# Optimization experiments

Measured on AMD Instinct MI355X. Metric: run time of the kernel, lower is better.

## Reference

```python
import jax, jax.numpy as jnp
import numpy as np

H = 4096      # hidden_size
NH = 32       # num heads
HD = H // NH  # head_dim = 128
I = 11008     # intermediate_size
T = 2048      # num tokens (single prompt sequence)
G = 128       # AWQ group size
EPS = 1e-6
ROPE_BASE = 10000.0


def _make_qlinear(key, k_in, n_out):
    k1, k2, k3 = jax.random.split(key, 3)
    qw = jax.random.randint(k1, (k_in, n_out), 0, 16, dtype=jnp.int32)
    qz = jax.random.randint(k2, (k_in // G, n_out), 0, 16, dtype=jnp.int32)
    scales = jax.random.uniform(k3, (k_in // G, n_out), dtype=jnp.float32) * 0.01 + 1e-3
    return qw, scales, qz


def setup_inputs() -> dict:
    key = jax.random.key(0)
    ks = jax.random.split(key, 8)
    inp = {
        "positions": jnp.arange(T, dtype=jnp.int64),
        "hidden_states": jax.random.normal(ks[0], (T, H), dtype=jnp.float32),
        "input_ln_w": jnp.ones((H,), dtype=jnp.float32),
        "post_ln_w": jnp.ones((H,), dtype=jnp.float32),
    }
    inp["qkv_qw"], inp["qkv_scales"], inp["qkv_qz"] = _make_qlinear(ks[1], H, 3 * H)
    inp["o_qw"], inp["o_scales"], inp["o_qz"] = _make_qlinear(ks[2], H, H)
    inp["gu_qw"], inp["gu_scales"], inp["gu_qz"] = _make_qlinear(ks[3], H, 2 * I)
    inp["down_qw"], inp["down_scales"], inp["down_qz"] = _make_qlinear(ks[4], I, H)
    return inp


def rms_norm(x, w):
    var = jnp.mean(x * x, axis=-1, keepdims=True)
    return x * jax.lax.rsqrt(var + EPS) * w


def awq_linear(x, qw, scales, qz):
    # dequant: (q - z) * scale, group-wise along K; then dense GEMM
    w = (qw.astype(scales.dtype) - jnp.repeat(qz.astype(scales.dtype), G, axis=0)) \
        * jnp.repeat(scales, G, axis=0)
    return x @ w


def apply_rope(x, positions):
    # x: [T, NH, HD], neox-style half rotation, rotary_dim = HD
    inv_freq = 1.0 / (ROPE_BASE ** (jnp.arange(0, HD, 2, dtype=jnp.float32) / HD))
    ang = positions.astype(jnp.float32)[:, None] * inv_freq  # [T, HD/2]
    cos = jnp.cos(ang)[:, None, :]
    sin = jnp.sin(ang)[:, None, :]
    x1, x2 = x[..., : HD // 2], x[..., HD // 2:]
    return jnp.concatenate([x1 * cos - x2 * sin, x2 * cos + x1 * sin], axis=-1)


def reference(positions, hidden_states, input_ln_w, post_ln_w,
              qkv_qw, qkv_scales, qkv_qz, o_qw, o_scales, o_qz,
              gu_qw, gu_scales, gu_qz, down_qw, down_scales, down_qz):
    residual = hidden_states
    x = rms_norm(hidden_states, input_ln_w)

    # attention
    qkv = awq_linear(x, qkv_qw, qkv_scales, qkv_qz)  # [T, 3H]
    q, k, v = jnp.split(qkv, 3, axis=-1)
    q = apply_rope(q.reshape(T, NH, HD), positions)
    k = apply_rope(k.reshape(T, NH, HD), positions)
    v = v.reshape(T, NH, HD)
    scale = HD ** -0.5
    scores = jnp.einsum('qhd,khd->hqk', q, k) * scale  # [NH, T, T]
    causal = jnp.tril(jnp.ones((T, T), dtype=bool))
    scores = jnp.where(causal[None], scores, jnp.finfo(scores.dtype).min)
    probs = jax.nn.softmax(scores, axis=-1)
    attn = jnp.einsum('hqk,khd->qhd', probs, v).reshape(T, H)
    attn_out = awq_linear(attn, o_qw, o_scales, o_qz)

    hidden = residual + attn_out
    residual = hidden
    x = rms_norm(hidden, post_ln_w)

    # MLP: gate_up -> silu(gate) * up -> down
    gate_up = awq_linear(x, gu_qw, gu_scales, gu_qz)  # [T, 2I]
    gate, up = jnp.split(gate_up, 2, axis=-1)
    x = jax.nn.silu(gate) * up
    x = awq_linear(x, down_qw, down_scales, down_qz)
    return residual + x
```

## Files before the change

### kernel.cpp

```cpp
#include <hip/hip_runtime.h>
#include <stdint.h>

#define T_SEQ 2048
#define HID 4096
#define NHEADS 32
#define I_FF 11008
#define QKV_N 12288
#define GU_N 22016

typedef unsigned short u16;
typedef unsigned int u32;
typedef __attribute__((ext_vector_type(4))) float f32x4;
typedef __attribute__((ext_vector_type(8))) __bf16 bf16x8;
typedef __attribute__((ext_vector_type(4))) u32 u32x4;
typedef __attribute__((ext_vector_type(2))) u32 u32x2;

__device__ __forceinline__ u16 f2bf(float f) {
  union { float f; u32 u; } v; v.f = f;
  u32 u = v.u;
  return (u16)((u + 0x7fffu + ((u >> 16) & 1u)) >> 16);
}
__device__ __forceinline__ float bf2f(u16 h) {
  union { u32 u; float f; } v; v.u = ((u32)h) << 16;
  return v.f;
}
__device__ __forceinline__ void split2(float x, u16& hi, u16& lo) {
  hi = f2bf(x);
  lo = f2bf(x - bf2f(hi));
}
__device__ __forceinline__ void split8(const float* v, u32x4& H, u32x4& L) {
#pragma unroll
  for (int j = 0; j < 4; j++) {
    u16 h0, l0, h1, l1;
    split2(v[2 * j], h0, l0);
    split2(v[2 * j + 1], h1, l1);
    H[j] = (u32)h0 | ((u32)h1 << 16);
    L[j] = (u32)l0 | ((u32)l1 << 16);
  }
}

__global__ __launch_bounds__(256) void pack_qw_kernel(
    const int* __restrict__ qw, u32* __restrict__ pw, int N) {
  int n = blockIdx.x * 256 + threadIdx.x;
  int oct = blockIdx.y;
  const int* src = qw + (size_t)oct * 8 * N + n;
  u32 v = 0;
#pragma unroll
  for (int j = 0; j < 8; j++)
    v |= ((u32)src[(size_t)j * N] & 15u) << (4 * j);
  pw[(size_t)oct * N + n] = v;
}

__global__ __launch_bounds__(256) void rmsnorm_kernel(
    const float* __restrict__ in, const float* __restrict__ w,
    u16* __restrict__ outh, u16* __restrict__ outl) {
  int row = blockIdx.x;
  const float* x = in + (size_t)row * HID;
  float4 vals[4];
  float ss = 0.f;
#pragma unroll
  for (int k = 0; k < 4; k++) {
    vals[k] = ((const float4*)x)[threadIdx.x + k * 256];
    ss += vals[k].x * vals[k].x + vals[k].y * vals[k].y +
          vals[k].z * vals[k].z + vals[k].w * vals[k].w;
  }
#pragma unroll
  for (int o = 1; o < 64; o <<= 1) ss += __shfl_xor(ss, o);
  __shared__ float red[4];
  if ((threadIdx.x & 63) == 0) red[threadIdx.x >> 6] = ss;
  __syncthreads();
  ss = red[0] + red[1] + red[2] + red[3];
  float rs = rsqrtf(ss * (1.f / HID) + 1e-6f);
#pragma unroll
  for (int k = 0; k < 4; k++) {
    int c4 = threadIdx.x + k * 256;
    float4 wv = ((const float4*)w)[c4];
    float o[4] = {vals[k].x * rs * wv.x, vals[k].y * rs * wv.y,
                  vals[k].z * rs * wv.z, vals[k].w * rs * wv.w};
    u32x2 H, L;
#pragma unroll
    for (int j = 0; j < 2; j++) {
      u16 h0, l0, h1, l1;
      split2(o[2 * j], h0, l0);
      split2(o[2 * j + 1], h1, l1);
      H[j] = (u32)h0 | ((u32)h1 << 16);
      L[j] = (u32)l0 | ((u32)l1 << 16);
    }
    *(u32x2*)(outh + (size_t)row * HID + c4 * 4) = H;
    *(u32x2*)(outl + (size_t)row * HID + c4 * 4) = L;
  }
}

template <bool RESID, bool OUTBF16, bool HILO>
__global__ __launch_bounds__(512) void awq_gemm_kernel(
    const u16* __restrict__ Ahg, const u16* __restrict__ Alg,
    const u32* __restrict__ pw, const float* __restrict__ scales,
    const int* __restrict__ qz, const float* __restrict__ resid,
    void* __restrict__ outp, int N, int K, int nstrips) {
  __shared__ u16 AhL[2][128][40];
  __shared__ u16 AlL[2][HILO ? 128 : 1][40];
  __shared__ u16 BqL[2][128][40];
  int tid = threadIdx.x;
  int lane = tid & 63;
  int wid = tid >> 6;
  int g16 = lane >> 4, l16 = lane & 15;
  int p = blockIdx.x;
  int xcd = p & 7;
  int idx = p >> 3;
  int s = idx >> 1;
  int mi = ((idx & 1) << 3) + xcd;
  if (s >= nstrips) return;
  int m0 = mi * 128;
  int n0 = s * 128;
  int wr = wid >> 1, wc = wid & 1;

  f32x4 acc[2][4] = {};
  float svold[4];

  int a_row = tid >> 2, a_kc = (tid & 3) * 8;
  const u16* aph = Ahg + (size_t)(m0 + a_row) * K + a_kc;
  const u16* apl = Alg + (size_t)(m0 + a_row) * K + a_kc;
  int b_n = tid & 127, b_kb = (tid >> 7) * 8;
  const u32* pwp = pw + (size_t)(tid >> 7) * N + n0 + b_n;
  const float* scp = scales + n0;
  const int* qzp = qz + n0 + b_n;

  int nsteps = K >> 5;

  u32x4 rah, ral;
  u32 rbp;

  auto load_step = [&](int ks) {
    int k0 = ks << 5;
    rah = *(const u32x4*)(aph + k0);
    if (HILO) ral = *(const u32x4*)(apl + k0);
    rbp = pwp[(size_t)(ks << 2) * N];
  };
  auto write_step = [&](int buf, int zq) {
    *(u32x4*)&AhL[buf][a_row][a_kc] = rah;
    if (HILO) *(u32x4*)&AlL[buf][a_row][a_kc] = ral;
    u32x4 w;
#pragma unroll
    for (int j = 0; j < 4; j++) {
      int q0 = (int)((rbp >> (8 * j)) & 15u) - zq;
      int q1 = (int)((rbp >> (8 * j + 4)) & 15u) - zq;
      u32 b0 = __builtin_bit_cast(u32, (float)q0);
      u32 b1 = __builtin_bit_cast(u32, (float)q1);
      w[j] = (b0 >> 16) | (b1 & 0xffff0000u);
    }
    *(u32x4*)&BqL[buf][b_n][b_kb] = w;
  };

  int zq = qzp[0];
  load_step(0);
  write_step(0, zq);
#pragma unroll
  for (int n = 0; n < 4; n++)
    svold[n] = scp[wc * 64 + n * 16 + l16];
  __syncthreads();

  int cur = 0;
  for (int ks = 0; ks < nsteps; ks++) {
    int nxt = ks + 1;
    if (nxt < nsteps) {
      if ((nxt & 3) == 0) zq = qzp[(size_t)(nxt >> 2) * N];
      load_step(nxt);
    }
    if (ks != 0 && (ks & 3) == 0) {
      int g = ks >> 2;
#pragma unroll
      for (int n = 0; n < 4; n++) {
        float svnew = scp[(size_t)g * N + wc * 64 + n * 16 + l16];
        float r = svold[n] * __builtin_amdgcn_rcpf(svnew);
        svold[n] = svnew;
#pragma unroll
        for (int m = 0; m < 2; m++)
#pragma unroll
          for (int i = 0; i < 4; i++) acc[m][n][i] *= r;
      }
    }
    bf16x8 bq[4];
#pragma unroll
    for (int n = 0; n < 4; n++)
      bq[n] = __builtin_bit_cast(bf16x8,
          *(const u32x4*)&BqL[cur][wc * 64 + n * 16 + l16][g16 * 8]);
#pragma unroll
    for (int m = 0; m < 2; m++) {
      bf16x8 ah = __builtin_bit_cast(bf16x8,
          *(const u32x4*)&AhL[cur][wr * 32 + m * 16 + l16][g16 * 8]);
      bf16x8 al;
      if (HILO)
        al = __builtin_bit_cast(bf16x8,
            *(const u32x4*)&AlL[cur][wr * 32 + m * 16 + l16][g16 * 8]);
#pragma unroll
      for (int n = 0; n < 4; n++) {
        if (HILO)
          acc[m][n] = __builtin_amdgcn_mfma_f32_16x16x32_bf16(al, bq[n], acc[m][n], 0, 0, 0);
        acc[m][n] = __builtin_amdgcn_mfma_f32_16x16x32_bf16(ah, bq[n], acc[m][n], 0, 0, 0);
      }
    }
    if (nxt < nsteps) write_step(cur ^ 1, zq);
    __syncthreads();
    cur ^= 1;
  }
#pragma unroll
  for (int n = 0; n < 4; n++)
#pragma unroll
    for (int m = 0; m < 2; m++)
#pragma unroll
      for (int i = 0; i < 4; i++) acc[m][n][i] *= svold[n];
#pragma unroll
  for (int m = 0; m < 2; m++) {
#pragma unroll
    for (int n = 0; n < 4; n++) {
#pragma unroll
      for (int r = 0; r < 4; r++) {
        int row = m0 + wr * 32 + m * 16 + g16 * 4 + r;
        int col = n0 + wc * 64 + n * 16 + l16;
        float v = acc[m][n][r];
        if (RESID) v += resid[(size_t)row * N + col];
        if (OUTBF16)
          ((u16*)outp)[(size_t)row * N + col] = f2bf(v);
        else
          ((float*)outp)[(size_t)row * N + col] = v;
      }
    }
  }
}

__global__ __launch_bounds__(256) void rope_kernel(float* __restrict__ qkv) {
  int t = blockIdx.x;
  __shared__ float cs[64], sn[64];
  if (threadIdx.x < 64) {
    int i = threadIdx.x;
    float freq = exp2f(-(float)i * (13.287712379549449f / 64.f));
    float ang = (float)t * freq;
    cs[i] = cosf(ang);
    sn[i] = sinf(ang);
  }
  __syncthreads();
#pragma unroll
  for (int it = 0; it < 16; it++) {
    int idx = threadIdx.x + it * 256;
    int part = idx >> 11;
    int rem = idx & 2047;
    int hh = rem >> 6, i = rem & 63;
    float* base = qkv + (size_t)t * QKV_N + (size_t)part * HID + hh * 128;
    float x1 = base[i], x2 = base[64 + i];
    float c = cs[i], s = sn[i];
    base[i] = x1 * c - x2 * s;
    base[64 + i] = x2 * c + x1 * s;
  }
}

__global__ __launch_bounds__(256) void transpose_v_kernel(
    const float* __restrict__ qkv, u16* __restrict__ vt) {
  __shared__ u16 tile[64][65];
  int tb = blockIdx.x;
  int cb = blockIdx.y;
  int tid = threadIdx.x;
  int r = tid >> 2, c16 = (tid & 3) * 16;
  const float* src = qkv + (size_t)(tb * 64 + r) * QKV_N + 2 * HID + cb * 64 + c16;
  float v[16];
  *(float4*)&v[0] = *(const float4*)(src);
  *(float4*)&v[4] = *(const float4*)(src + 4);
  *(float4*)&v[8] = *(const float4*)(src + 8);
  *(float4*)&v[12] = *(const float4*)(src + 12);
#pragma unroll
  for (int i = 0; i < 16; i++) tile[r][c16 + i] = f2bf(v[i]);
  __syncthreads();
  int ocol = tid >> 2, tchunk = (tid & 3) * 16;
  u16 vbuf[16];
#pragma unroll
  for (int i = 0; i < 16; i++) vbuf[i] = tile[tchunk + i][ocol];
  u16* dst = vt + (size_t)(cb * 64 + ocol) * T_SEQ + tb * 64 + tchunk;
  *(u32x4*)dst = *(u32x4*)&vbuf[0];
  *(u32x4*)(dst + 8) = *(u32x4*)&vbuf[8];
}

__global__ __launch_bounds__(256) void attn_kernel(
    const float* __restrict__ qkv, const u16* __restrict__ vt,
    u16* __restrict__ outh, u16* __restrict__ outl) {
  constexpr float SCALE = 0.08838834764831845f;
  __shared__ u16 Kh[32][136], Kl[32][136];
  __shared__ u16 Vt_lds[128][40];
  __shared__ u16 P_lds[4][16][40];
  int tid = threadIdx.x;
  int wid = tid >> 6, lane = tid & 63;
  int g16 = lane >> 4, l16 = lane & 15;
  int h = blockIdx.x & 31;
  int qt = blockIdx.x >> 5;
  int qb = qt * 64;

  bf16x8 qh[4], ql[4];
  {
    const float* qsrc = qkv + (size_t)(qb + wid * 16 + l16) * QKV_N + h * 128;
#pragma unroll
    for (int ds = 0; ds < 4; ds++) {
      float v[8];
      *(float4*)&v[0] = *(const float4*)(qsrc + ds * 32 + g16 * 8);
      *(float4*)&v[4] = *(const float4*)(qsrc + ds * 32 + g16 * 8 + 4);
      u32x4 H, L;
      split8(v, H, L);
      qh[ds] = __builtin_bit_cast(bf16x8, H);
      ql[ds] = __builtin_bit_cast(bf16x8, L);
    }
  }
  f32x4 oacc[8] = {};
  float mrun[4] = {-1e30f, -1e30f, -1e30f, -1e30f};
  float lrun[4] = {0.f, 0.f, 0.f, 0.f};

  int st_k = tid >> 3, st_d = (tid & 7) * 16;
  int sv_d = tid >> 1, sv_k = (tid & 1) * 16;

  int ktiles = (qb + 64) >> 5;
  for (int kt = 0; kt < ktiles; kt++) {
    __syncthreads();
    {
      const float* src = qkv + (size_t)(kt * 32 + st_k) * QKV_N + HID + h * 128 + st_d;
      float v[16];
      *(float4*)&v[0] = *(const float4*)(src);
      *(float4*)&v[4] = *(const float4*)(src + 4);
      *(float4*)&v[8] = *(const float4*)(src + 8);
      *(float4*)&v[12] = *(const float4*)(src + 12);
      u32x4 H, L;
      split8(&v[0], H, L);
      *(u32x4*)&Kh[st_k][st_d] = H;
      *(u32x4*)&Kl[st_k][st_d] = L;
      split8(&v[8], H, L);
      *(u32x4*)&Kh[st_k][st_d + 8] = H;
      *(u32x4*)&Kl[st_k][st_d + 8] = L;
    }
    {
      const u16* src = vt + (size_t)(h * 128 + sv_d) * T_SEQ + kt * 32 + sv_k;
      *(u32x4*)&Vt_lds[sv_d][sv_k] = *(const u32x4*)src;
      *(u32x4*)&Vt_lds[sv_d][sv_k + 8] = *(const u32x4*)(src + 8);
    }
    __syncthreads();
    f32x4 sacc[2] = {};
#pragma unroll
    for (int kb = 0; kb < 2; kb++)
#pragma unroll
      for (int ds = 0; ds < 4; ds++) {
        bf16x8 kfh = __builtin_bit_cast(bf16x8,
            *(const u32x4*)&Kh[kb * 16 + l16][ds * 32 + g16 * 8]);
        bf16x8 kfl = __builtin_bit_cast(bf16x8,
            *(const u32x4*)&Kl[kb * 16 + l16][ds * 32 + g16 * 8]);
        sacc[kb] = __builtin_amdgcn_mfma_f32_16x16x32_bf16(qh[ds], kfh, sacc[kb], 0, 0, 0);
        sacc[kb] = __builtin_amdgcn_mfma_f32_16x16x32_bf16(ql[ds], kfh, sacc[kb], 0, 0, 0);
        sacc[kb] = __builtin_amdgcn_mfma_f32_16x16x32_bf16(qh[ds], kfl, sacc[kb], 0, 0, 0);
      }
    float p0v[4], p1v[4];
#pragma unroll
    for (int r = 0; r < 4; r++) {
      int qrow = qb + wid * 16 + g16 * 4 + r;
      bool msk0 = (kt * 32 + l16) > qrow;
      bool msk1 = (kt * 32 + 16 + l16) > qrow;
      float s0 = msk0 ? -1e30f : sacc[0][r] * SCALE;
      float s1 = msk1 ? -1e30f : sacc[1][r] * SCALE;
      float tm = fmaxf(s0, s1);
      tm = fmaxf(tm, __shfl_xor(tm, 1));
      tm = fmaxf(tm, __shfl_xor(tm, 2));
      tm = fmaxf(tm, __shfl_xor(tm, 4));
      tm = fmaxf(tm, __shfl_xor(tm, 8));
      float mnew = fmaxf(mrun[r], tm);
      float fac = __expf(mrun[r] - mnew);
      float p0 = msk0 ? 0.f : __expf(s0 - mnew);
      float p1 = msk1 ? 0.f : __expf(s1 - mnew);
      float ts = p0 + p1;
      ts += __shfl_xor(ts, 1);
      ts += __shfl_xor(ts, 2);
      ts += __shfl_xor(ts, 4);
      ts += __shfl_xor(ts, 8);
      lrun[r] = lrun[r] * fac + ts;
      mrun[r] = mnew;
      p0v[r] = p0; p1v[r] = p1;
#pragma unroll
      for (int db = 0; db < 8; db++) oacc[db][r] *= fac;
    }
#pragma unroll
    for (int r = 0; r < 4; r++) {
      P_lds[wid][g16 * 4 + r][l16] = f2bf(p0v[r]);
      P_lds[wid][g16 * 4 + r][16 + l16] = f2bf(p1v[r]);
    }
    __syncthreads();
    bf16x8 pa = __builtin_bit_cast(bf16x8, *(const u32x4*)&P_lds[wid][l16][g16 * 8]);
#pragma unroll
    for (int db = 0; db < 8; db++) {
      bf16x8 vb = __builtin_bit_cast(bf16x8,
          *(const u32x4*)&Vt_lds[db * 16 + l16][g16 * 8]);
      oacc[db] = __builtin_amdgcn_mfma_f32_16x16x32_bf16(pa, vb, oacc[db], 0, 0, 0);
    }
  }
#pragma unroll
  for (int r = 0; r < 4; r++) {
    int qrow = qb + wid * 16 + g16 * 4 + r;
    float inv = 1.f / lrun[r];
#pragma unroll
    for (int db = 0; db < 8; db++) {
      float v = oacc[db][r] * inv;
      u16 h16, l16v;
      split2(v, h16, l16v);
      size_t idx = (size_t)qrow * HID + h * 128 + db * 16 + l16;
      outh[idx] = h16;
      outl[idx] = l16v;
    }
  }
}

__global__ __launch_bounds__(256) void silu_mul_kernel(
    const u16* __restrict__ gu, u16* __restrict__ acth, u16* __restrict__ actl) {
  size_t e = ((size_t)blockIdx.x * 256 + threadIdx.x) * 8;
  size_t row = e / I_FF;
  int col = (int)(e % I_FF);
  const u16* gp = gu + row * GU_N + col;
  u32x4 gv = *(const u32x4*)gp;
  u32x4 uv = *(const u32x4*)(gp + I_FF);
  float o[8];
#pragma unroll
  for (int j = 0; j < 4; j++) {
    float g0 = bf2f((u16)(gv[j] & 0xffff)), g1 = bf2f((u16)(gv[j] >> 16));
    float u0 = bf2f((u16)(uv[j] & 0xffff)), u1 = bf2f((u16)(uv[j] >> 16));
    o[2 * j] = g0 / (1.f + __expf(-g0)) * u0;
    o[2 * j + 1] = g1 / (1.f + __expf(-g1)) * u1;
  }
  u32x4 H, L;
  split8(o, H, L);
  *(u32x4*)(acth + row * I_FF + col) = H;
  *(u32x4*)(actl + row * I_FF + col) = L;
}

extern "C" void kernel_launch(void* const* d_in, const int* in_sizes, int n_in,
                              void* d_out, int out_size, void* d_ws, size_t ws_size,
                              hipStream_t stream) {
  const float* hs    = (const float*)d_in[1];
  const float* ln1   = (const float*)d_in[2];
  const float* ln2   = (const float*)d_in[3];
  const int* qkv_qw  = (const int*)d_in[4];
  const float* qkv_s = (const float*)d_in[5];
  const int* qkv_z   = (const int*)d_in[6];
  const int* o_qw    = (const int*)d_in[7];
  const float* o_s   = (const float*)d_in[8];
  const int* o_z     = (const int*)d_in[9];
  const int* gu_qw   = (const int*)d_in[10];
  const float* gu_s  = (const float*)d_in[11];
  const int* gu_z    = (const int*)d_in[12];
  const int* dn_qw   = (const int*)d_in[13];
  const float* dn_s  = (const float*)d_in[14];
  const int* dn_z    = (const int*)d_in[15];

  char* ws = (char*)d_ws;
  u16*   xnh    = (u16*)(ws);
  u16*   xnl    = (u16*)(ws + (size_t)16777216);
  float* qkv    = (float*)(ws + (size_t)33554432);
  u16*   vt     = (u16*)(ws + (size_t)134217728);
  float* hidden = (float*)(ws + (size_t)150994944);
  u16*   gup    = (u16*)(ws + (size_t)184549376);
  u16*   attnh  = xnh;
  u16*   attnl  = xnl;
  u16*   acth   = (u16*)qkv;
  u16*   actl   = (u16*)qkv + (size_t)T_SEQ * I_FF;
  u32* pk_gup = (u32*)gup;
  u32* pk_qkv = (u32*)qkv;

  auto gemm_grid = [](int N) { return 16 * (N / 128); };

  rmsnorm_kernel<<<T_SEQ, 256, 0, stream>>>(hs, ln1, xnh, xnl);
  pack_qw_kernel<<<dim3(QKV_N / 256, HID / 8), 256, 0, stream>>>(qkv_qw, pk_gup, QKV_N);
  awq_gemm_kernel<false, false, true><<<gemm_grid(QKV_N), 512, 0, stream>>>(
      xnh, xnl, pk_gup, qkv_s, qkv_z, nullptr, qkv, QKV_N, HID, QKV_N / 128);
  rope_kernel<<<T_SEQ, 256, 0, stream>>>(qkv);
  transpose_v_kernel<<<dim3(T_SEQ / 64, HID / 64), 256, 0, stream>>>(qkv, vt);
  attn_kernel<<<NHEADS * (T_SEQ / 64), 256, 0, stream>>>(qkv, vt, attnh, attnl);
  pack_qw_kernel<<<dim3(HID / 256, HID / 8), 256, 0, stream>>>(o_qw, pk_gup, HID);
  awq_gemm_kernel<true, false, false><<<gemm_grid(HID), 512, 0, stream>>>(
      attnh, attnl, pk_gup, o_s, o_z, hs, hidden, HID, HID, HID / 128);
  rmsnorm_kernel<<<T_SEQ, 256, 0, stream>>>(hidden, ln2, xnh, xnl);
  pack_qw_kernel<<<dim3(GU_N / 256, HID / 8), 256, 0, stream>>>(gu_qw, pk_qkv, GU_N);
  awq_gemm_kernel<false, true, false><<<gemm_grid(GU_N), 512, 0, stream>>>(
      xnh, xnl, pk_qkv, gu_s, gu_z, nullptr, gup, GU_N, HID, GU_N / 128);
  silu_mul_kernel<<<(T_SEQ * (size_t)I_FF / 8 / 256), 256, 0, stream>>>(gup, acth, actl);
  pack_qw_kernel<<<dim3(HID / 256, I_FF / 8), 256, 0, stream>>>(dn_qw, pk_gup, HID);
  awq_gemm_kernel<true, false, false><<<gemm_grid(HID), 512, 0, stream>>>(
      acth, actl, pk_gup, dn_s, dn_z, hidden, (float*)d_out, HID, I_FF, HID / 128);
}
```

Measured before the change: 1.811 ms.

## Add 128x256-tile AWQ GEMM for single-bf16 projections and drop unused lo activations

Adds a new AWQ GEMM kernel with a 128x256 output tile (each wave computes 64x64) for the o_proj, gate_up and down projections. The bigger tile doubles B-side work per block and raises MFMA work per LDS load, cutting how often A tiles are re-read. silu_mul now writes only the high bf16 part, since those GEMMs never read the low part. The original 128x128 kernel is reduced to always-on hi/lo for QKV, and the packed gate_up weights move to a separate workspace offset. The larger tile halves the grid for N=4096 to 256 blocks, which may leave compute units underused and raises register pressure.

```diff
diff --git a/kernel.cpp b/kernel.cpp
--- a/kernel.cpp
+++ b/kernel.cpp
@@ -36,6 +36,16 @@
     split2(v[2 * j + 1], h1, l1);
     H[j] = (u32)h0 | ((u32)h1 << 16);
     L[j] = (u32)l0 | ((u32)l1 << 16);
+  }
+}
+__device__ __forceinline__ void dq8(u32 rbp, int zq, u32x4& w) {
+#pragma unroll
+  for (int j = 0; j < 4; j++) {
+    int q0 = (int)((rbp >> (8 * j)) & 15u) - zq;
+    int q1 = (int)((rbp >> (8 * j + 4)) & 15u) - zq;
+    u32 b0 = __builtin_bit_cast(u32, (float)q0);
+    u32 b1 = __builtin_bit_cast(u32, (float)q1);
+    w[j] = (b0 >> 16) | (b1 & 0xffff0000u);
   }
 }
 
@@ -91,14 +101,14 @@
   }
 }
 
-template <bool RESID, bool OUTBF16, bool HILO>
+template <bool RESID, bool OUTBF16>
 __global__ __launch_bounds__(512) void awq_gemm_kernel(
     const u16* __restrict__ Ahg, const u16* __restrict__ Alg,
     const u32* __restrict__ pw, const float* __restrict__ scales,
     const int* __restrict__ qz, const float* __restrict__ resid,
     void* __restrict__ outp, int N, int K, int nstrips) {
   __shared__ u16 AhL[2][128][40];
-  __shared__ u16 AlL[2][HILO ? 128 : 1][40];
+  __shared__ u16 AlL[2][128][40];
   __shared__ u16 BqL[2][128][40];
   int tid = threadIdx.x;
   int lane = tid & 63;
@@ -133,21 +143,14 @@
   auto load_step = [&](int ks) {
     int k0 = ks << 5;
     rah = *(const u32x4*)(aph + k0);
-    if (HILO) ral = *(const u32x4*)(apl + k0);
+    ral = *(const u32x4*)(apl + k0);
     rbp = pwp[(size_t)(ks << 2) * N];
   };
   auto write_step = [&](int buf, int zq) {
     *(u32x4*)&AhL[buf][a_row][a_kc] = rah;
-    if (HILO) *(u32x4*)&AlL[buf][a_row][a_kc] = ral;
+    *(u32x4*)&AlL[buf][a_row][a_kc] = ral;
     u32x4 w;
-#pragma unroll
-    for (int j = 0; j < 4; j++) {
-      int q0 = (int)((rbp >> (8 * j)) & 15u) - zq;
-      int q1 = (int)((rbp >> (8 * j + 4)) & 15u) - zq;
-      u32 b0 = __builtin_bit_cast(u32, (float)q0);
-      u32 b1 = __builtin_bit_cast(u32, (float)q1);
-      w[j] = (b0 >> 16) | (b1 & 0xffff0000u);
-    }
+    dq8(rbp, zq, w);
     *(u32x4*)&BqL[buf][b_n][b_kb] = w;
   };
 
@@ -188,14 +191,11 @@
     for (int m = 0; m < 2; m++) {
       bf16x8 ah = __builtin_bit_cast(bf16x8,
           *(const u32x4*)&AhL[cur][wr * 32 + m * 16 + l16][g16 * 8]);
-      bf16x8 al;
-      if (HILO)
-        al = __builtin_bit_cast(bf16x8,
-            *(const u32x4*)&AlL[cur][wr * 32 + m * 16 + l16][g16 * 8]);
+      bf16x8 al = __builtin_bit_cast(bf16x8,
+          *(const u32x4*)&AlL[cur][wr * 32 + m * 16 + l16][g16 * 8]);
 #pragma unroll
       for (int n = 0; n < 4; n++) {
-        if (HILO)
-          acc[m][n] = __builtin_amdgcn_mfma_f32_16x16x32_bf16(al, bq[n], acc[m][n], 0, 0, 0);
+        acc[m][n] = __builtin_amdgcn_mfma_f32_16x16x32_bf16(al, bq[n], acc[m][n], 0, 0, 0);
         acc[m][n] = __builtin_amdgcn_mfma_f32_16x16x32_bf16(ah, bq[n], acc[m][n], 0, 0, 0);
       }
     }
@@ -216,6 +216,131 @@
 #pragma unroll
       for (int r = 0; r < 4; r++) {
         int row = m0 + wr * 32 + m * 16 + g16 * 4 + r;
+        int col = n0 + wc * 64 + n * 16 + l16;
+        float v = acc[m][n][r];
+        if (RESID) v += resid[(size_t)row * N + col];
+        if (OUTBF16)
+          ((u16*)outp)[(size_t)row * N + col] = f2bf(v);
+        else
+          ((float*)outp)[(size_t)row * N + col] = v;
+      }
+    }
+  }
+}
+
+template <bool RESID, bool OUTBF16>
+__global__ __launch_bounds__(512) void awq_gemm256_kernel(
+    const u16* __restrict__ Ahg,
+    const u32* __restrict__ pw, const float* __restrict__ scales,
+    const int* __restrict__ qz, const float* __restrict__ resid,
+    void* __restrict__ outp, int N, int K, int nstrips) {
+  __shared__ u16 AhL[2][128][40];
+  __shared__ u16 BqL[2][256][40];
+  int tid = threadIdx.x;
+  int lane = tid & 63;
+  int wid = tid >> 6;
+  int g16 = lane >> 4, l16 = lane & 15;
+  int p = blockIdx.x;
+  int xcd = p & 7;
+  int idx = p >> 3;
+  int s = idx >> 1;
+  int mi = ((idx & 1) << 3) + xcd;
+  if (s >= nstrips) return;
+  int m0 = mi * 128;
+  int n0 = s * 256;
+  int wr = wid >> 2, wc = wid & 3;
+
+  f32x4 acc[4][4] = {};
+  float svold[4];
+
+  int a_row = tid >> 2, a_kc = (tid & 3) * 8;
+  const u16* aph = Ahg + (size_t)(m0 + a_row) * K + a_kc;
+  int b_n = tid & 255;
+  int b_oct = (tid >> 8) * 2;
+  int b_kb = b_oct * 8;
+  const u32* pwp = pw + (size_t)b_oct * N + n0 + b_n;
+  const float* scp = scales + n0;
+  const int* qzp = qz + n0 + b_n;
+
+  int nsteps = K >> 5;
+
+  u32x4 rah;
+  u32 rb0, rb1;
+
+  auto load_step = [&](int ks) {
+    int k0 = ks << 5;
+    rah = *(const u32x4*)(aph + k0);
+    const u32* q = pwp + (size_t)(ks << 2) * N;
+    rb0 = q[0];
+    rb1 = q[N];
+  };
+  auto write_step = [&](int buf, int zq) {
+    *(u32x4*)&AhL[buf][a_row][a_kc] = rah;
+    u32x4 w0, w1;
+    dq8(rb0, zq, w0);
+    dq8(rb1, zq, w1);
+    *(u32x4*)&BqL[buf][b_n][b_kb] = w0;
+    *(u32x4*)&BqL[buf][b_n][b_kb + 8] = w1;
+  };
+
+  int zq = qzp[0];
+  load_step(0);
+  write_step(0, zq);
+#pragma unroll
+  for (int n = 0; n < 4; n++)
+    svold[n] = scp[wc * 64 + n * 16 + l16];
+  __syncthreads();
+
+  int cur = 0;
+  for (int ks = 0; ks < nsteps; ks++) {
+    int nxt = ks + 1;
+    if (nxt < nsteps) {
+      if ((nxt & 3) == 0) zq = qzp[(size_t)(nxt >> 2) * N];
+      load_step(nxt);
+    }
+    if (ks != 0 && (ks & 3) == 0) {
+      int g = ks >> 2;
+#pragma unroll
+      for (int n = 0; n < 4; n++) {
+        float svnew = scp[(size_t)g * N + wc * 64 + n * 16 + l16];
+        float r = svold[n] * __builtin_amdgcn_rcpf(svnew);
+        svold[n] = svnew;
+#pragma unroll
+        for (int m = 0; m < 4; m++)
+#pragma unroll
+          for (int i = 0; i < 4; i++) acc[m][n][i] *= r;
+      }
+    }
+    bf16x8 bq[4];
+#pragma unroll
+    for (int n = 0; n < 4; n++)
+      bq[n] = __builtin_bit_cast(bf16x8,
+          *(const u32x4*)&BqL[cur][wc * 64 + n * 16 + l16][g16 * 8]);
+#pragma unroll
+    for (int m = 0; m < 4; m++) {
+      bf16x8 ah = __builtin_bit_cast(bf16x8,
+          *(const u32x4*)&AhL[cur][wr * 64 + m * 16 + l16][g16 * 8]);
+#pragma unroll
+      for (int n = 0; n < 4; n++)
+        acc[m][n] = __builtin_amdgcn_mfma_f32_16x16x32_bf16(ah, bq[n], acc[m][n], 0, 0, 0);
+    }
+    if (nxt < nsteps) write_step(cur ^ 1, zq);
+    __syncthreads();
+    cur ^= 1;
+  }
+#pragma unroll
+  for (int n = 0; n < 4; n++)
+#pragma unroll
+    for (int m = 0; m < 4; m++)
+#pragma unroll
+      for (int i = 0; i < 4; i++) acc[m][n][i] *= svold[n];
+#pragma unroll
+  for (int m = 0; m < 4; m++) {
+#pragma unroll
+    for (int n = 0; n < 4; n++) {
+#pragma unroll
+      for (int r = 0; r < 4; r++) {
+        int row = m0 + wr * 64 + m * 16 + g16 * 4 + r;
         int col = n0 + wc * 64 + n * 16 + l16;
         float v = acc[m][n][r];
         if (RESID) v += resid[(size_t)row * N + col];
@@ -409,25 +534,23 @@
 }
 
 __global__ __launch_bounds__(256) void silu_mul_kernel(
-    const u16* __restrict__ gu, u16* __restrict__ acth, u16* __restrict__ actl) {
+    const u16* __restrict__ gu, u16* __restrict__ acth) {
   size_t e = ((size_t)blockIdx.x * 256 + threadIdx.x) * 8;
   size_t row = e / I_FF;
   int col = (int)(e % I_FF);
   const u16* gp = gu + row * GU_N + col;
   u32x4 gv = *(const u32x4*)gp;
   u32x4 uv = *(const u32x4*)(gp + I_FF);
-  float o[8];
+  u32x4 H;
 #pragma unroll
   for (int j = 0; j < 4; j++) {
     float g0 = bf2f((u16)(gv[j] & 0xffff)), g1 = bf2f((u16)(gv[j] >> 16));
     float u0 = bf2f((u16)(uv[j] & 0xffff)), u1 = bf2f((u16)(uv[j] >> 16));
-    o[2 * j] = g0 / (1.f + __expf(-g0)) * u0;
-    o[2 * j + 1] = g1 / (1.f + __expf(-g1)) * u1;
-  }
-  u32x4 H, L;
-  split8(o, H, L);
+    float o0 = g0 / (1.f + __expf(-g0)) * u0;
+    float o1 = g1 / (1.f + __expf(-g1)) * u1;
+    H[j] = (u32)f2bf(o0) | ((u32)f2bf(o1) << 16);
+  }
   *(u32x4*)(acth + row * I_FF + col) = H;
-  *(u32x4*)(actl + row * I_FF + col) = L;
 }
 
 extern "C" void kernel_launch(void* const* d_in, const int* in_sizes, int n_in,
@@ -459,28 +582,28 @@
   u16*   attnh  = xnh;
   u16*   attnl  = xnl;
   u16*   acth   = (u16*)qkv;
-  u16*   actl   = (u16*)qkv + (size_t)T_SEQ * I_FF;
   u32* pk_gup = (u32*)gup;
-  u32* pk_qkv = (u32*)qkv;
-
-  auto gemm_grid = [](int N) { return 16 * (N / 128); };
+  u32* pk_qkv = (u32*)((char*)qkv + (size_t)50331648);
+
+  auto grid128 = [](int N) { return 16 * (N / 128); };
+  auto grid256 = [](int N) { return 16 * (N / 256); };
 
   rmsnorm_kernel<<<T_SEQ, 256, 0, stream>>>(hs, ln1, xnh, xnl);
   pack_qw_kernel<<<dim3(QKV_N / 256, HID / 8), 256, 0, stream>>>(qkv_qw, pk_gup, QKV_N);
-  awq_gemm_kernel<false, false, true><<<gemm_grid(QKV_N), 512, 0, stream>>>(
+  awq_gemm_kernel<false, false><<<grid128(QKV_N), 512, 0, stream>>>(
       xnh, xnl, pk_gup, qkv_s, qkv_z, nullptr, qkv, QKV_N, HID, QKV_N / 128);
   rope_kernel<<<T_SEQ, 256, 0, stream>>>(qkv);
   transpose_v_kernel<<<dim3(T_SEQ / 64, HID / 64), 256, 0, stream>>>(qkv, vt);
   attn_kernel<<<NHEADS * (T_SEQ / 64), 256, 0, stream>>>(qkv, vt, attnh, attnl);
   pack_qw_kernel<<<dim3(HID / 256, HID / 8), 256, 0, stream>>>(o_qw, pk_gup, HID);
-  awq_gemm_kernel<true, false, false><<<gemm_grid(HID), 512, 0, stream>>>(
-      attnh, attnl, pk_gup, o_s, o_z, hs, hidden, HID, HID, HID / 128);
+  awq_gemm256_kernel<true, false><<<grid256(HID), 512, 0, stream>>>(
+      attnh, pk_gup, o_s, o_z, hs, hidden, HID, HID, HID / 256);
   rmsnorm_kernel<<<T_SEQ, 256, 0, stream>>>(hidden, ln2, xnh, xnl);
   pack_qw_kernel<<<dim3(GU_N / 256, HID / 8), 256, 0, stream>>>(gu_qw, pk_qkv, GU_N);
-  awq_gemm_kernel<false, true, false><<<gemm_grid(GU_N), 512, 0, stream>>>(
-      xnh, xnl, pk_qkv, gu_s, gu_z, nullptr, gup, GU_N, HID, GU_N / 128);
-  silu_mul_kernel<<<(T_SEQ * (size_t)I_FF / 8 / 256), 256, 0, stream>>>(gup, acth, actl);
+  awq_gemm256_kernel<false, true><<<grid256(GU_N), 512, 0, stream>>>(
+      xnh, pk_qkv, gu_s, gu_z, nullptr, gup, GU_N, HID, GU_N / 256);
+  silu_mul_kernel<<<(T_SEQ * (size_t)I_FF / 8 / 256), 256, 0, stream>>>(gup, acth);
   pack_qw_kernel<<<dim3(HID / 256, I_FF / 8), 256, 0, stream>>>(dn_qw, pk_gup, HID);
-  awq_gemm_kernel<true, false, false><<<gemm_grid(HID), 512, 0, stream>>>(
-      acth, actl, pk_gup, dn_s, dn_z, hidden, (float*)d_out, HID, I_FF, HID / 128);
-}
+  awq_gemm256_kernel<true, false><<<grid256(HID), 512, 0, stream>>>(
+      acth, pk_gup, dn_s, dn_z, hidden, (float*)d_out, HID, I_FF, HID / 256);
+}
```

After: 1.804 ms. Within noise of the previous version (-0.4%).

## Drop hi/lo bf16 split and widen AWQ GEMM tile to 128x256

Applied to the files above, without the earlier changes.

Removes the two-term bf16 (hi+lo) activation representation everywhere. RMSNorm, attention and SiLU now write a single bf16 tensor, and the QKV GEMM issues one MFMA per product instead of two. The AWQ GEMM tile grows from 128x128 to 128x256, with each thread dequantizing two packed words per step, to increase B-tile reuse and halve the number of blocks. Costs are lower QKV precision and larger per-wave accumulators, which may affect occupancy; the workspace layout is adjusted to fit.

```diff
diff --git a/kernel.cpp b/kernel.cpp
--- a/kernel.cpp
+++ b/kernel.cpp
@@ -38,6 +38,16 @@
     L[j] = (u32)l0 | ((u32)l1 << 16);
   }
 }
+__device__ __forceinline__ void dq8(u32 rbp, int zq, u32x4& w) {
+#pragma unroll
+  for (int j = 0; j < 4; j++) {
+    int q0 = (int)((rbp >> (8 * j)) & 15u) - zq;
+    int q1 = (int)((rbp >> (8 * j + 4)) & 15u) - zq;
+    u32 b0 = __builtin_bit_cast(u32, (float)q0);
+    u32 b1 = __builtin_bit_cast(u32, (float)q1);
+    w[j] = (b0 >> 16) | (b1 & 0xffff0000u);
+  }
+}
 
 __global__ __launch_bounds__(256) void pack_qw_kernel(
     const int* __restrict__ qw, u32* __restrict__ pw, int N) {
@@ -53,7 +63,7 @@
 
 __global__ __launch_bounds__(256) void rmsnorm_kernel(
     const float* __restrict__ in, const float* __restrict__ w,
-    u16* __restrict__ outh, u16* __restrict__ outl) {
+    u16* __restrict__ outh) {
   int row = blockIdx.x;
   const float* x = in + (size_t)row * HID;
   float4 vals[4];
@@ -77,29 +87,21 @@
     float4 wv = ((const float4*)w)[c4];
     float o[4] = {vals[k].x * rs * wv.x, vals[k].y * rs * wv.y,
                   vals[k].z * rs * wv.z, vals[k].w * rs * wv.w};
-    u32x2 H, L;
-#pragma unroll
-    for (int j = 0; j < 2; j++) {
-      u16 h0, l0, h1, l1;
-      split2(o[2 * j], h0, l0);
-      split2(o[2 * j + 1], h1, l1);
-      H[j] = (u32)h0 | ((u32)h1 << 16);
-      L[j] = (u32)l0 | ((u32)l1 << 16);
-    }
+    u32x2 H;
+    H[0] = (u32)f2bf(o[0]) | ((u32)f2bf(o[1]) << 16);
+    H[1] = (u32)f2bf(o[2]) | ((u32)f2bf(o[3]) << 16);
     *(u32x2*)(outh + (size_t)row * HID + c4 * 4) = H;
-    *(u32x2*)(outl + (size_t)row * HID + c4 * 4) = L;
-  }
-}
-
-template <bool RESID, bool OUTBF16, bool HILO>
-__global__ __launch_bounds__(512) void awq_gemm_kernel(
-    const u16* __restrict__ Ahg, const u16* __restrict__ Alg,
+  }
+}
+
+template <bool RESID, bool OUTBF16>
+__global__ __launch_bounds__(512) void awq_gemm256_kernel(
+    const u16* __restrict__ Ahg,
     const u32* __restrict__ pw, const float* __restrict__ scales,
     const int* __restrict__ qz, const float* __restrict__ resid,
     void* __restrict__ outp, int N, int K, int nstrips) {
   __shared__ u16 AhL[2][128][40];
-  __shared__ u16 AlL[2][HILO ? 128 : 1][40];
-  __shared__ u16 BqL[2][128][40];
+  __shared__ u16 BqL[2][256][40];
   int tid = threadIdx.x;
   int lane = tid & 63;
   int wid = tid >> 6;
@@ -111,44 +113,40 @@
   int mi = ((idx & 1) << 3) + xcd;
   if (s >= nstrips) return;
   int m0 = mi * 128;
-  int n0 = s * 128;
-  int wr = wid >> 1, wc = wid & 1;
-
-  f32x4 acc[2][4] = {};
+  int n0 = s * 256;
+  int wr = wid >> 2, wc = wid & 3;
+
+  f32x4 acc[4][4] = {};
   float svold[4];
 
   int a_row = tid >> 2, a_kc = (tid & 3) * 8;
   const u16* aph = Ahg + (size_t)(m0 + a_row) * K + a_kc;
-  const u16* apl = Alg + (size_t)(m0 + a_row) * K + a_kc;
-  int b_n = tid & 127, b_kb = (tid >> 7) * 8;
-  const u32* pwp = pw + (size_t)(tid >> 7) * N + n0 + b_n;
+  int b_n = tid & 255;
+  int b_oct = (tid >> 8) * 2;
+  int b_kb = b_oct * 8;
+  const u32* pwp = pw + (size_t)b_oct * N + n0 + b_n;
   const float* scp = scales + n0;
   const int* qzp = qz + n0 + b_n;
 
   int nsteps = K >> 5;
 
-  u32x4 rah, ral;
-  u32 rbp;
+  u32x4 rah;
+  u32 rb0, rb1;
 
   auto load_step = [&](int ks) {
     int k0 = ks << 5;
     rah = *(const u32x4*)(aph + k0);
-    if (HILO) ral = *(const u32x4*)(apl + k0);
-    rbp = pwp[(size_t)(ks << 2) * N];
+    const u32* q = pwp + (size_t)(ks << 2) * N;
+    rb0 = q[0];
+    rb1 = q[N];
   };
   auto write_step = [&](int buf, int zq) {
     *(u32x4*)&AhL[buf][a_row][a_kc] = rah;
-    if (HILO) *(u32x4*)&AlL[buf][a_row][a_kc] = ral;
-    u32x4 w;
-#pragma unroll
-    for (int j = 0; j < 4; j++) {
-      int q0 = (int)((rbp >> (8 * j)) & 15u) - zq;
-      int q1 = (int)((rbp >> (8 * j + 4)) & 15u) - zq;
-      u32 b0 = __builtin_bit_cast(u32, (float)q0);
-      u32 b1 = __builtin_bit_cast(u32, (float)q1);
-      w[j] = (b0 >> 16) | (b1 & 0xffff0000u);
-    }
-    *(u32x4*)&BqL[buf][b_n][b_kb] = w;
+    u32x4 w0, w1;
+    dq8(rb0, zq, w0);
+    dq8(rb1, zq, w1);
+    *(u32x4*)&BqL[buf][b_n][b_kb] = w0;
+    *(u32x4*)&BqL[buf][b_n][b_kb + 8] = w1;
   };
 
   int zq = qzp[0];
@@ -174,7 +172,7 @@
         float r = svold[n] * __builtin_amdgcn_rcpf(svnew);
         svold[n] = svnew;
 #pragma unroll
-        for (int m = 0; m < 2; m++)
+        for (int m = 0; m < 4; m++)
 #pragma unroll
           for (int i = 0; i < 4; i++) acc[m][n][i] *= r;
       }
@@ -185,19 +183,12 @@
       bq[n] = __builtin_bit_cast(bf16x8,
           *(const u32x4*)&BqL[cur][wc * 64 + n * 16 + l16][g16 * 8]);
 #pragma unroll
-    for (int m = 0; m < 2; m++) {
+    for (int m = 0; m < 4; m++) {
       bf16x8 ah = __builtin_bit_cast(bf16x8,
-          *(const u32x4*)&AhL[cur][wr * 32 + m * 16 + l16][g16 * 8]);
-      bf16x8 al;
-      if (HILO)
-        al = __builtin_bit_cast(bf16x8,
-            *(const u32x4*)&AlL[cur][wr * 32 + m * 16 + l16][g16 * 8]);
-#pragma unroll
-      for (int n = 0; n < 4; n++) {
-        if (HILO)
-          acc[m][n] = __builtin_amdgcn_mfma_f32_16x16x32_bf16(al, bq[n], acc[m][n], 0, 0, 0);
+          *(const u32x4*)&AhL[cur][wr * 64 + m * 16 + l16][g16 * 8]);
+#pragma unroll
+      for (int n = 0; n < 4; n++)
         acc[m][n] = __builtin_amdgcn_mfma_f32_16x16x32_bf16(ah, bq[n], acc[m][n], 0, 0, 0);
-      }
     }
     if (nxt < nsteps) write_step(cur ^ 1, zq);
     __syncthreads();
@@ -206,16 +197,16 @@
 #pragma unroll
   for (int n = 0; n < 4; n++)
 #pragma unroll
-    for (int m = 0; m < 2; m++)
+    for (int m = 0; m < 4; m++)
 #pragma unroll
       for (int i = 0; i < 4; i++) acc[m][n][i] *= svold[n];
 #pragma unroll
-  for (int m = 0; m < 2; m++) {
+  for (int m = 0; m < 4; m++) {
 #pragma unroll
     for (int n = 0; n < 4; n++) {
 #pragma unroll
       for (int r = 0; r < 4; r++) {
-        int row = m0 + wr * 32 + m * 16 + g16 * 4 + r;
+        int row = m0 + wr * 64 + m * 16 + g16 * 4 + r;
         int col = n0 + wc * 64 + n * 16 + l16;
         float v = acc[m][n][r];
         if (RESID) v += resid[(size_t)row * N + col];
@@ -280,7 +271,7 @@
 
 __global__ __launch_bounds__(256) void attn_kernel(
     const float* __restrict__ qkv, const u16* __restrict__ vt,
-    u16* __restrict__ outh, u16* __restrict__ outl) {
+    u16* __restrict__ outh) {
   constexpr float SCALE = 0.08838834764831845f;
   __shared__ u16 Kh[32][136], Kl[32][136];
   __shared__ u16 Vt_lds[128][40];
@@ -397,37 +388,30 @@
     int qrow = qb + wid * 16 + g16 * 4 + r;
     float inv = 1.f / lrun[r];
 #pragma unroll
-    for (int db = 0; db < 8; db++) {
-      float v = oacc[db][r] * inv;
-      u16 h16, l16v;
-      split2(v, h16, l16v);
-      size_t idx = (size_t)qrow * HID + h * 128 + db * 16 + l16;
-      outh[idx] = h16;
-      outl[idx] = l16v;
-    }
+    for (int db = 0; db < 8; db++)
+      outh[(size_t)qrow * HID + h * 128 + db * 16 + l16] =
+          f2bf(oacc[db][r] * inv);
   }
 }
 
 __global__ __launch_bounds__(256) void silu_mul_kernel(
-    const u16* __restrict__ gu, u16* __restrict__ acth, u16* __restrict__ actl) {
+    const u16* __restrict__ gu, u16* __restrict__ acth) {
   size_t e = ((size_t)blockIdx.x * 256 + threadIdx.x) * 8;
   size_t row = e / I_FF;
   int col = (int)(e % I_FF);
   const u16* gp = gu + row * GU_N + col;
   u32x4 gv = *(const u32x4*)gp;
   u32x4 uv = *(const u32x4*)(gp + I_FF);
-  float o[8];
+  u32x4 H;
 #pragma unroll
   for (int j = 0; j < 4; j++) {
     float g0 = bf2f((u16)(gv[j] & 0xffff)), g1 = bf2f((u16)(gv[j] >> 16));
     float u0 = bf2f((u16)(uv[j] & 0xffff)), u1 = bf2f((u16)(uv[j] >> 16));
-    o[2 * j] = g0 / (1.f + __expf(-g0)) * u0;
-    o[2 * j + 1] = g1 / (1.f + __expf(-g1)) * u1;
-  }
-  u32x4 H, L;
-  split8(o, H, L);
+    float o0 = g0 / (1.f + __expf(-g0)) * u0;
+    float o1 = g1 / (1.f + __expf(-g1)) * u1;
+    H[j] = (u32)f2bf(o0) | ((u32)f2bf(o1) << 16);
+  }
   *(u32x4*)(acth + row * I_FF + col) = H;
-  *(u32x4*)(actl + row * I_FF + col) = L;
 }
 
 extern "C" void kernel_launch(void* const* d_in, const int* in_sizes, int n_in,
@@ -451,36 +435,33 @@
 
   char* ws = (char*)d_ws;
   u16*   xnh    = (u16*)(ws);
-  u16*   xnl    = (u16*)(ws + (size_t)16777216);
   float* qkv    = (float*)(ws + (size_t)33554432);
   u16*   vt     = (u16*)(ws + (size_t)134217728);
   float* hidden = (float*)(ws + (size_t)150994944);
   u16*   gup    = (u16*)(ws + (size_t)184549376);
   u16*   attnh  = xnh;
-  u16*   attnl  = xnl;
   u16*   acth   = (u16*)qkv;
-  u16*   actl   = (u16*)qkv + (size_t)T_SEQ * I_FF;
   u32* pk_gup = (u32*)gup;
-  u32* pk_qkv = (u32*)qkv;
-
-  auto gemm_grid = [](int N) { return 16 * (N / 128); };
-
-  rmsnorm_kernel<<<T_SEQ, 256, 0, stream>>>(hs, ln1, xnh, xnl);
+  u32* pk_qkv = (u32*)((char*)qkv + (size_t)50331648);
+
+  auto grid256 = [](int N) { return 16 * (N / 256); };
+
+  rmsnorm_kernel<<<T_SEQ, 256, 0, stream>>>(hs, ln1, xnh);
   pack_qw_kernel<<<dim3(QKV_N / 256, HID / 8), 256, 0, stream>>>(qkv_qw, pk_gup, QKV_N);
-  awq_gemm_kernel<false, false, true><<<gemm_grid(QKV_N), 512, 0, stream>>>(
-      xnh, xnl, pk_gup, qkv_s, qkv_z, nullptr, qkv, QKV_N, HID, QKV_N / 128);
+  awq_gemm256_kernel<false, false><<<grid256(QKV_N), 512, 0, stream>>>(
+      xnh, pk_gup, qkv_s, qkv_z, nullptr, qkv, QKV_N, HID, QKV_N / 256);
   rope_kernel<<<T_SEQ, 256, 0, stream>>>(qkv);
   transpose_v_kernel<<<dim3(T_SEQ / 64, HID / 64), 256, 0, stream>>>(qkv, vt);
-  attn_kernel<<<NHEADS * (T_SEQ / 64), 256, 0, stream>>>(qkv, vt, attnh, attnl);
+  attn_kernel<<<NHEADS * (T_SEQ / 64), 256, 0, stream>>>(qkv, vt, attnh);
   pack_qw_kernel<<<dim3(HID / 256, HID / 8), 256, 0, stream>>>(o_qw, pk_gup, HID);
-  awq_gemm_kernel<true, false, false><<<gemm_grid(HID), 512, 0, stream>>>(
-      attnh, attnl, pk_gup, o_s, o_z, hs, hidden, HID, HID, HID / 128);
-  rmsnorm_kernel<<<T_SEQ, 256, 0, stream>>>(hidden, ln2, xnh, xnl);
+  awq_gemm256_kernel<true, false><<<grid256(HID), 512, 0, stream>>>(
+      attnh, pk_gup, o_s, o_z, hs, hidden, HID, HID, HID / 256);
+  rmsnorm_kernel<<<T_SEQ, 256, 0, stream>>>(hidden, ln2, xnh);
   pack_qw_kernel<<<dim3(GU_N / 256, HID / 8), 256, 0, stream>>>(gu_qw, pk_qkv, GU_N);
-  awq_gemm_kernel<false, true, false><<<gemm_grid(GU_N), 512, 0, stream>>>(
-      xnh, xnl, pk_qkv, gu_s, gu_z, nullptr, gup, GU_N, HID, GU_N / 128);
-  silu_mul_kernel<<<(T_SEQ * (size_t)I_FF / 8 / 256), 256, 0, stream>>>(gup, acth, actl);
+  awq_gemm256_kernel<false, true><<<grid256(GU_N), 512, 0, stream>>>(
+      xnh, pk_qkv, gu_s, gu_z, nullptr, gup, GU_N, HID, GU_N / 256);
+  silu_mul_kernel<<<(T_SEQ * (size_t)I_FF / 8 / 256), 256, 0, stream>>>(gup, acth);
   pack_qw_kernel<<<dim3(HID / 256, I_FF / 8), 256, 0, stream>>>(dn_qw, pk_gup, HID);
-  awq_gemm_kernel<true, false, false><<<gemm_grid(HID), 512, 0, stream>>>(
-      acth, actl, pk_gup, dn_s, dn_z, hidden, (float*)d_out, HID, I_FF, HID / 128);
-}
+  awq_gemm256_kernel<true, false><<<grid256(HID), 512, 0, stream>>>(
+      acth, pk_gup, dn_s, dn_z, hidden, (float*)d_out, HID, I_FF, HID / 256);
+}
```

New measurement: 1.634 ms. 1.11x faster.
